# Performance work log

Measured on AMD Instinct MI355X. Metric: run time of the kernel, lower is better.

Reference implementation:

```python
import jax, jax.numpy as jnp
import numpy as np

B, T, C, H = 4, 2048, 1024, 16
HD = C // H


def setup_inputs() -> dict:
    key = jax.random.key(0)
    ks = jax.random.split(key, 9)
    s = 1.0 / np.sqrt(C)
    return {
        "x": jax.random.normal(ks[0], (B, T, C), dtype=jnp.float32),
        "Wk": jax.random.uniform(ks[1], (C, C), jnp.float32, -s, s),
        "bk": jax.random.uniform(ks[2], (C,), jnp.float32, -s, s),
        "Wq": jax.random.uniform(ks[3], (C, C), jnp.float32, -s, s),
        "bq": jax.random.uniform(ks[4], (C,), jnp.float32, -s, s),
        "Wv": jax.random.uniform(ks[5], (C, C), jnp.float32, -s, s),
        "bv": jax.random.uniform(ks[6], (C,), jnp.float32, -s, s),
        "Wp": jax.random.uniform(ks[7], (C, C), jnp.float32, -s, s),
        "bp": jax.random.uniform(ks[8], (C,), jnp.float32, -s, s),
        "padding_mask": jnp.ones((B, T), dtype=jnp.int32),
    }


def reference(x, Wk, bk, Wq, bq, Wv, bv, Wp, bp, padding_mask):
    # torch nn.Linear: y = x @ W.T + b  (W is [out, in])
    def split_heads(t):  # [B,T,C] -> [B,H,T,HD]
        return t.reshape(B, T, H, HD).transpose(0, 2, 1, 3)

    k = split_heads(x @ Wk.T + bk)
    q = split_heads(x @ Wq.T + bq)
    v = split_heads(x @ Wv.T + bv)

    scale = 1.0 / jnp.sqrt(jnp.float32(HD))
    att = jnp.einsum("bhqd,bhkd->bhqk", q, k) * scale  # [B,H,T,T]

    causal = jnp.tril(jnp.ones((T, T), dtype=bool))  # [T,T]
    pad = (padding_mask != 0)[:, None, None, :]       # [B,1,1,T]
    mask = causal[None, None, :, :] & pad
    att = jnp.where(mask, att, -jnp.inf)
    att = jax.nn.softmax(att, axis=-1)

    y = jnp.einsum("bhqk,bhkd->bhqd", att, v)  # [B,H,T,HD]
    y = y.transpose(0, 2, 1, 3).reshape(B, T, C)
    return y @ Wp.T + bp
```

## Files before the change

### kernel.cpp

```cpp
#include <hip/hip_runtime.h>
#include <hip/hip_bf16.h>
#include <math.h>
#include <stdint.h>

#define BB 4
#define TT 2048
#define CC 1024
#define HH 16
#define HD 64
#define MM (BB*TT)
#define NQT2 16
#define SCQ 0.180336878f

using f32x2  = __attribute__((ext_vector_type(2))) float;
using f32x4  = __attribute__((ext_vector_type(4))) float;
using f32x16 = __attribute__((ext_vector_type(16))) float;
using i32x4  = __attribute__((ext_vector_type(4))) int;
using bf16x4 = __attribute__((ext_vector_type(4))) __bf16;
using bf16x8 = __attribute__((ext_vector_type(8))) __bf16;

__device__ __forceinline__ float fast_exp2(float x) {
  return __builtin_amdgcn_exp2f(x);
}

__device__ __forceinline__ int cvt_pk_bf16(float lo, float hi_) {
  int r;
  asm("v_cvt_pk_bf16_f32 %0, %1, %2" : "=v"(r) : "v"(lo), "v"(hi_));
  return r;
}

__device__ __forceinline__ f32x2 max2(f32x2 a, f32x2 b) {
  return __builtin_elementwise_max(a, b);
}

__device__ __forceinline__ void gload_lds16(const void* g, void* l) {
  __builtin_amdgcn_global_load_lds(
      (__attribute__((address_space(1))) void*)(void*)(g),
      (__attribute__((address_space(3))) void*)(l), 16, 0, 0);
}

__global__ __launch_bounds__(256)
void cvt_f32_bf16(const float* __restrict__ s, __bf16* __restrict__ d, int n4) {
  int i = blockIdx.x * 256 + threadIdx.x;
  if (i >= n4) return;
  float4 v = ((const float4*)s)[i];
  bf16x4 o;
  o[0] = (__bf16)v.x; o[1] = (__bf16)v.y; o[2] = (__bf16)v.z; o[3] = (__bf16)v.w;
  *(bf16x4*)(d + (size_t)i * 4) = o;
}

__global__ __launch_bounds__(256)
void cvt_w4(const float* __restrict__ Wq, const float* __restrict__ Wk,
            const float* __restrict__ Wv, const float* __restrict__ Wp,
            __bf16* __restrict__ wqkv, __bf16* __restrict__ wpb) {
  int which = blockIdx.y;
  const float* s = which == 0 ? Wq : which == 1 ? Wk : which == 2 ? Wv : Wp;
  __bf16* d = which == 3 ? wpb : wqkv + (size_t)which * CC * CC;
  float sc = which == 0 ? SCQ : 1.f;
  int i = blockIdx.x * 256 + threadIdx.x;
  float4 v = ((const float4*)s)[i];
  bf16x4 o;
  o[0] = (__bf16)(v.x * sc); o[1] = (__bf16)(v.y * sc);
  o[2] = (__bf16)(v.z * sc); o[3] = (__bf16)(v.w * sc);
  *(bf16x4*)(d + (size_t)i * 4) = o;
}

#define WAITV0 asm volatile("s_waitcnt vmcnt(0)" ::: "memory")
#define SB0    __builtin_amdgcn_sched_barrier(0)

__global__ __launch_bounds__(256, 2)
void gemm_qkv(const __bf16* __restrict__ A, const __bf16* __restrict__ Bm,
              const float* __restrict__ b0, const float* __restrict__ b1,
              const float* __restrict__ b2, __bf16* __restrict__ out,
              __bf16* __restrict__ vt) {
  __shared__ __bf16 U[8448];
  __bf16* As = U;
  __bf16* Bs = U + 4096;
  const int tid = threadIdx.x;
  const int wid = tid >> 6, lane = tid & 63;
  const int g = lane >> 4, lq = lane & 15;
  const int bx0 = blockIdx.x;
  const int bx = (bx0 & 7) * 192 + (bx0 >> 3);
  const int bm = bx / 24, bn = bx % 24;
  const int brow = bm << 7, bcol = bn << 7;
  const int wr = (wid >> 1) << 6, wc = (wid & 1) << 6;

  const int c0 = tid, c1 = tid + 256;
  const int r0 = c0 >> 2, s0_ = (((c0 & 3) - (r0 >> 1)) & 3) << 4;
  const int r1 = c1 >> 2, s1_ = (((c1 & 3) - (r1 >> 1)) & 3) << 4;

  f32x4 acc[4][4] = {};

  for (int kt = 0; kt < CC; kt += 32) {
    __syncthreads();
    gload_lds16((const char*)A + (size_t)(brow + r0) * 2048 + kt * 2 + s0_,
                (char*)As + c0 * 16);
    gload_lds16((const char*)A + (size_t)(brow + r1) * 2048 + kt * 2 + s1_,
                (char*)As + c1 * 16);
    gload_lds16((const char*)Bm + (size_t)(bcol + r0) * 2048 + kt * 2 + s0_,
                (char*)Bs + c0 * 16);
    gload_lds16((const char*)Bm + (size_t)(bcol + r1) * 2048 + kt * 2 + s1_,
                (char*)Bs + c1 * 16);
    __syncthreads();
    bf16x8 av[4], bv[4];
#pragma unroll
    for (int m = 0; m < 4; ++m) {
      int row = wr + m * 16 + lq;
      int sl = (g + (row >> 1)) & 3;
      av[m] = *(const bf16x8*)((const char*)As + row * 64 + sl * 16);
    }
#pragma unroll
    for (int n = 0; n < 4; ++n) {
      int row = wc + n * 16 + lq;
      int sl = (g + (row >> 1)) & 3;
      bv[n] = *(const bf16x8*)((const char*)Bs + row * 64 + sl * 16);
    }
#pragma unroll
    for (int m = 0; m < 4; ++m)
#pragma unroll
      for (int n = 0; n < 4; ++n)
        acc[m][n] = __builtin_amdgcn_mfma_f32_16x16x32_bf16(av[m], bv[n], acc[m][n], 0, 0, 0);
  }

  const int proj = bn >> 3;
  if (proj < 2) {
    const float* bias = proj == 0 ? b0 : b1;
    const float bsc = proj == 0 ? SCQ : 1.f;
#pragma unroll
    for (int n = 0; n < 4; ++n) {
      int col = bcol + wc + n * 16 + lq;
      int cw = col & (CC - 1);
      float bb = bias[cw] * bsc;
      int h_ = cw >> 6, d_ = cw & (HD - 1);
#pragma unroll
      for (int m = 0; m < 4; ++m) {
        int row0 = brow + wr + m * 16 + g * 4;
#pragma unroll
        for (int i = 0; i < 4; ++i) {
          int row = row0 + i;
          int b_ = row >> 11, t_ = row & (TT - 1);
          out[((size_t)proj << 23) +
              ((((size_t)b_ * HH + h_) * TT + t_) << 6) + d_] =
              (__bf16)(acc[m][n][i] + bb);
        }
      }
    }
  } else {
    __syncthreads();
    __bf16* lt = U;
    const int cv0 = (bn & 7) << 7;
    const int b_ = brow >> 11, t0 = brow & (TT - 1);
    const int hbase = (bn & 7) << 1;
    const int rd_d = tid >> 2, rd_tb = (tid & 3) << 5;
#pragma unroll
    for (int cc = 0; cc < 2; ++cc) {
      if ((wid & 1) == cc) {
#pragma unroll
        for (int n = 0; n < 4; ++n) {
          int c = (n << 4) + lq;
          float bb = b2[cv0 + (cc << 6) + c];
#pragma unroll
          for (int m = 0; m < 4; ++m) {
            int r = wr + (m << 4) + (g << 2);
            bf16x4 pk;
#pragma unroll
            for (int i = 0; i < 4; ++i)
              pk[i] = (__bf16)(acc[m][n][i] + bb);
            *(bf16x4*)(lt + c * 130 + r) = pk;
          }
        }
      }
      __syncthreads();
      __bf16* dst = vt + (((size_t)((b_ * HH + hbase + cc) * HD + rd_d)) << 11)
                       + t0 + rd_tb;
      const __bf16* srcl = lt + rd_d * 130 + rd_tb;
#pragma unroll
      for (int j = 0; j < 4; ++j)
        *(bf16x8*)(dst + j * 8) = *(const bf16x8*)(srcl + j * 8);
      __syncthreads();
    }
  }
}

__global__ __launch_bounds__(256, 2)
void gemm_proj(const __bf16* __restrict__ A, const __bf16* __restrict__ Bm,
               const float* __restrict__ bias, float* __restrict__ out,
               int M, int N, int K) {
  __shared__ __bf16 As[128 * 32];
  __shared__ __bf16 Bs[128 * 32];
  const int tid = threadIdx.x;
  const int wid = tid >> 6, lane = tid & 63;
  const int g = lane >> 4, lq = lane & 15;
  const int nbn = N >> 7;
  int bx = blockIdx.x;
  const int nb = gridDim.x;
  if ((nb & 7) == 0) { const int q = nb >> 3; bx = (bx & 7) * q + (bx >> 3); }
  const int brow = (bx / nbn) << 7;
  const int bcol = (bx % nbn) << 7;
  const int wr = (wid >> 1) << 6, wc = (wid & 1) << 6;

  f32x4 acc[4][4] = {};

  const int o0 = wid * 2048 + lane * 16;
  for (int kt = 0; kt < K; kt += 32) {
    __syncthreads();
#pragma unroll
    for (int j = 0; j < 2; ++j) {
      int o = o0 + j * 1024;
      int row = o >> 6, colb = o & 63;
      gload_lds16((const char*)A + ((size_t)(brow + row) * K + kt) * 2 + colb,
                  (char*)As + o);
      gload_lds16((const char*)Bm + ((size_t)(bcol + row) * K + kt) * 2 + colb,
                  (char*)Bs + o);
    }
    __syncthreads();
    bf16x8 av[4], bv[4];
#pragma unroll
    for (int m = 0; m < 4; ++m)
      av[m] = *(const bf16x8*)(As + (wr + m * 16 + lq) * 32 + g * 8);
#pragma unroll
    for (int n = 0; n < 4; ++n)
      bv[n] = *(const bf16x8*)(Bs + (wc + n * 16 + lq) * 32 + g * 8);
#pragma unroll
    for (int m = 0; m < 4; ++m)
#pragma unroll
      for (int n = 0; n < 4; ++n)
        acc[m][n] = __builtin_amdgcn_mfma_f32_16x16x32_bf16(av[m], bv[n], acc[m][n], 0, 0, 0);
  }

#pragma unroll
  for (int m = 0; m < 4; ++m) {
#pragma unroll
    for (int n = 0; n < 4; ++n) {
      int col = bcol + wc + n * 16 + lq;
      float bb = bias[col];
      int row0 = brow + wr + m * 16 + g * 4;
#pragma unroll
      for (int i = 0; i < 4; ++i)
        out[(size_t)(row0 + i) * N + col] = acc[m][n][i] + bb;
    }
  }
}

__global__ __launch_bounds__(256, 4)
void attn_fwd(const __bf16* __restrict__ Q, const __bf16* __restrict__ K,
              const __bf16* __restrict__ Vt, const int* __restrict__ pm,
              __bf16* __restrict__ Y) {
  __shared__ __bf16 Ks[2][64 * 64];
  __shared__ __bf16 Vs[2][64 * 64];
  __shared__ int flg;
  const int tid = threadIdx.x, wid = tid >> 6, lane = tid & 63;
  const int l31 = lane & 31, hi = lane >> 5;
  const int bx = blockIdx.x;
  const int bh = bx & 63, jj = bx >> 6;
  const int qi = 15 - (4 * (jj >> 2) + ((jj + (jj >> 2)) & 3));
  const int b_ = bh >> 4, h_ = bh & 15;
  const __bf16* Qb = Q + (size_t)bh * TT * HD;
  const __bf16* Kb = K + (size_t)bh * TT * HD;
  const __bf16* Vb = Vt + (size_t)bh * HD * TT;
  const int* pmb = pm + b_ * TT;

  const int so = tid * 16;
  const int srow = tid >> 3;
  const int scol = (so & 127) ^ ((srow & 7) << 4);

  const int q0 = qi << 7;
  const int qw = q0 + wid * 32;
  const int ntiles = 2 * qi + 2;
  const int sw0 = (l31 & 7) << 4;

  bf16x8 qf[4];
#pragma unroll
  for (int s = 0; s < 4; ++s)
    qf[s] = *(const bf16x8*)(Qb + (size_t)(qw + l31) * HD + s * 16 + hi * 8);
  SB0;

  int4 pa4 = ((const int4*)pmb)[tid];
  int4 pb4 = ((const int4*)pmb)[tid + 256];
  bool okp = pa4.x && pa4.y && pa4.z && pa4.w &&
             pb4.x && pb4.y && pb4.z && pb4.w;
  if (tid == 0) flg = 1;
  __syncthreads();
  if (!okp) flg = 0;

  {
    char* kd = (char*)&Ks[0][0] + so;
    char* vd = (char*)&Vs[0][0] + so;
#pragma unroll
    for (int j = 0; j < 2; ++j) {
      gload_lds16((const char*)Kb + (size_t)(srow + 32 * j) * 128 + scol,
                  kd + j * 4096);
      gload_lds16((const char*)Vb + (size_t)(srow + 32 * j) * (TT * 2) + scol,
                  vd + j * 4096);
    }
  }
  __syncthreads();
  const bool allones = (flg != 0);

  f32x16 o0 = {}, o1 = {};
  f32x16 vzero = {};
  float lsum = 0.f;
  float m = -INFINITY;

  int cur = 0;
#pragma unroll 1
  for (int t = 0; t < ntiles; ++t) {
    const int kv0 = t << 6;
    WAITV0;
    __builtin_amdgcn_s_barrier(); SB0;
    if (t + 1 < ntiles) {
      char* kd = (char*)&Ks[0][0] + (cur ^ 1) * 8192 + so;
      char* vd = (char*)&Vs[0][0] + (cur ^ 1) * 8192 + so;
      const size_t nk = (size_t)(kv0 + 64);
#pragma unroll
      for (int j = 0; j < 2; ++j) {
        gload_lds16((const char*)Kb + (nk + srow + 32 * j) * 128 + scol,
                    kd + j * 4096);
        gload_lds16((const char*)Vb + (size_t)(srow + 32 * j) * (TT * 2) +
                        nk * 2 + scol,
                    vd + j * 4096);
      }
    }

    unsigned long long bits = ~0ull;
    if (__builtin_expect(!allones, 0))
      bits = __ballot(pmb[kv0 + lane] != 0);

    if (kv0 <= qw + 31) {
      const char* VsC = (const char*)&Vs[0][0] + cur * 8192;

#pragma unroll
      for (int h = 0; h < 2; ++h) {
        const int kvh = kv0 + 32 * h;
        if (kvh <= qw + 31) {
          const char* KsC =
              (const char*)&Ks[0][0] + cur * 8192 + (32 * h + l31) * 128;
          f32x16 S;
          __builtin_amdgcn_s_setprio(1);
          {
            bf16x8 k0 = *(const bf16x8*)(KsC + ((16 * hi) ^ sw0));
            S = __builtin_amdgcn_mfma_f32_32x32x16_bf16(k0, qf[0], vzero, 0, 0, 0);
          }
#pragma unroll
          for (int s = 1; s < 4; ++s) {
            bf16x8 kf = *(const bf16x8*)(KsC + ((32 * s + 16 * hi) ^ sw0));
            S = __builtin_amdgcn_mfma_f32_32x32x16_bf16(kf, qf[s], S, 0, 0, 0);
          }
          __builtin_amdgcn_s_setprio(0);

          if (__builtin_expect(bits != ~0ull, 0)) {
#pragma unroll
            for (int r = 0; r < 16; ++r) {
              const int c = (r & 3) + 8 * (r >> 2);
              if (!((bits >> (32 * h + c + 4 * hi)) & 1ull)) S[r] = -INFINITY;
            }
          }
          if (kvh + 31 > qw) {
            const int thr = qw + l31 - kvh - 4 * hi;
#pragma unroll
            for (int r = 0; r < 16; ++r) {
              const int c = (r & 3) + 8 * (r >> 2);
              S[r] = (c <= thr) ? S[r] : -INFINITY;
            }
          }

          f32x2 x0 = {S[0], S[1]},  x1 = {S[2], S[3]};
          f32x2 x2 = {S[4], S[5]},  x3 = {S[6], S[7]};
          f32x2 x4 = {S[8], S[9]},  x5 = {S[10], S[11]};
          f32x2 x6 = {S[12], S[13]}, x7 = {S[14], S[15]};
          x0 = max2(x0, x4); x1 = max2(x1, x5);
          x2 = max2(x2, x6); x3 = max2(x3, x7);
          x0 = max2(x0, x2); x1 = max2(x1, x3);
          x0 = max2(x0, x1);
          float pmax = fmaxf(x0[0], x0[1]);
          if (!__all(pmax <= m + 8.f)) {
            float nm = fmaxf(pmax, __shfl_xor(pmax, 32));
            float mn = fmaxf(m, nm);
            float c = fast_exp2(m - mn);
            m = mn;
            lsum *= c;
#pragma unroll
            for (int r = 0; r < 16; ++r) {
              float cr = __shfl(c, (r & 3) + 8 * (r >> 2) + 4 * hi);
              o0[r] *= cr;
              o1[r] *= cr;
            }
          }

          const f32x2 mm = {m, m};
#pragma unroll
          for (int r = 0; r < 16; r += 2) {
            f32x2 u = {S[r], S[r + 1]};
            u -= mm;
            S[r] = fast_exp2(u[0]);
            S[r + 1] = fast_exp2(u[1]);
          }
          {
            f32x2 u0 = {S[0], S[1]},  u1 = {S[2], S[3]};
            f32x2 u2 = {S[4], S[5]},  u3 = {S[6], S[7]};
            f32x2 u4 = {S[8], S[9]},  u5 = {S[10], S[11]};
            f32x2 u6 = {S[12], S[13]}, u7 = {S[14], S[15]};
            u0 += u4; u1 += u5; u2 += u6; u3 += u7;
            u0 += u2; u1 += u3;
            u0 += u1;
            lsum += u0[0] + u0[1];
          }

          __builtin_amdgcn_s_setprio(1);
#pragma unroll
          for (int s = 0; s < 2; ++s) {
            int A0 = cvt_pk_bf16(S[8 * s + 0], S[8 * s + 1]);
            int A1 = cvt_pk_bf16(S[8 * s + 2], S[8 * s + 3]);
            int B0 = cvt_pk_bf16(S[8 * s + 4], S[8 * s + 5]);
            int B1 = cvt_pk_bf16(S[8 * s + 6], S[8 * s + 7]);
            int s0 = hi ? A0 : B0, s1 = hi ? A1 : B1;
            int e0 = __shfl_xor(s0, 32), e1 = __shfl_xor(s1, 32);
            i32x4 wv;
            wv[0] = hi ? e0 : A0;
            wv[1] = hi ? e1 : A1;
            wv[2] = hi ? B0 : e0;
            wv[3] = hi ? B1 : e1;
            bf16x8 pa = __builtin_bit_cast(bf16x8, wv);
            const int co = 64 * h + 32 * s + 16 * hi;
            bf16x8 v0 = *(const bf16x8*)(VsC + l31 * 128 + (co ^ sw0));
            bf16x8 v1 = *(const bf16x8*)(VsC + (32 + l31) * 128 + (co ^ sw0));
            o0 = __builtin_amdgcn_mfma_f32_32x32x16_bf16(pa, v0, o0, 0, 0, 0);
            o1 = __builtin_amdgcn_mfma_f32_32x32x16_bf16(pa, v1, o1, 0, 0, 0);
          }
          __builtin_amdgcn_s_setprio(0);
        }
      }
    }
    SB0;
    cur ^= 1;
  }

  float linv = 1.f / (lsum + __shfl_xor(lsum, 32));
#pragma unroll
  for (int r = 0; r < 16; ++r) {
    const int crow = (r & 3) + 8 * (r >> 2) + 4 * hi;
    float ir = __shfl(linv, crow);
    const int qrow = qw + crow;
    __bf16* yp = Y + ((size_t)(b_ * TT + qrow)) * CC + h_ * HD + l31;
    yp[0]  = (__bf16)(o0[r] * ir);
    yp[32] = (__bf16)(o1[r] * ir);
  }
}

extern "C" void kernel_launch(void* const* d_in, const int* in_sizes, int n_in,
                              void* d_out, int out_size, void* d_ws, size_t ws_size,
                              hipStream_t stream) {
  (void)in_sizes; (void)n_in; (void)out_size; (void)ws_size;
  const float* x  = (const float*)d_in[0];
  const float* Wk = (const float*)d_in[1];
  const float* bk = (const float*)d_in[2];
  const float* Wq = (const float*)d_in[3];
  const float* bq = (const float*)d_in[4];
  const float* Wv = (const float*)d_in[5];
  const float* bv = (const float*)d_in[6];
  const float* Wp = (const float*)d_in[7];
  const float* bp = (const float*)d_in[8];
  const int* pmask = (const int*)d_in[9];

  char* ws = (char*)d_ws;
  const size_t MB = 1024 * 1024;
  __bf16* xb   = (__bf16*)(ws);
  __bf16* wqkv = (__bf16*)(ws + 16 * MB);
  __bf16* wpb  = (__bf16*)(ws + 22 * MB);
  __bf16* qb   = (__bf16*)(ws + 24 * MB);
  __bf16* kb   = qb + ((size_t)1 << 23);
  __bf16* vtb  = (__bf16*)(ws + 56 * MB);
  __bf16* yb   = xb;

  int n4 = (MM * CC) / 4;
  cvt_f32_bf16<<<(n4 + 255) / 256, 256, 0, stream>>>(x, xb, n4);
  cvt_w4<<<dim3((CC * CC / 4) / 256, 4), 256, 0, stream>>>(
      Wq, Wk, Wv, Wp, wqkv, wpb);

  gemm_qkv<<<(MM / 128) * (3 * CC / 128), 256, 0, stream>>>(
      xb, wqkv, bq, bk, bv, qb, vtb);

  attn_fwd<<<NQT2 * BB * HH, 256, 0, stream>>>(qb, kb, vtb, pmask, yb);

  gemm_proj<<<(MM / 128) * (CC / 128), 256, 0, stream>>>(
      yb, wpb, bp, (float*)d_out, MM, CC, CC);
}
```

Before: 174.6 us.

## Double-buffer LDS tiles in QKV and projection GEMMs with a single barrier per step

Both GEMM kernels now use two LDS buffers per operand. The next K-slice is issued with direct global-to-LDS loads while MFMAs run on the current one, and each iteration needs only one wait-and-barrier instead of two __syncthreads. The projection GEMM also adopts the swizzled LDS layout and block-index remap from the QKV kernel, and its dimensions are hardcoded. LDS use doubles to 32KB per block, which may affect occupancy and leaves less margin for the epilogue that reuses shared memory.

New measurement: 170.2 us. 2.6% less time.

```diff
diff --git a/kernel.cpp b/kernel.cpp
--- a/kernel.cpp
+++ b/kernel.cpp
@@ -66,6 +66,7 @@
 }
 
 #define WAITV0 asm volatile("s_waitcnt vmcnt(0)" ::: "memory")
+#define BARR   __builtin_amdgcn_s_barrier()
 #define SB0    __builtin_amdgcn_sched_barrier(0)
 
 __global__ __launch_bounds__(256, 2)
@@ -73,9 +74,8 @@
               const float* __restrict__ b0, const float* __restrict__ b1,
               const float* __restrict__ b2, __bf16* __restrict__ out,
               __bf16* __restrict__ vt) {
-  __shared__ __bf16 U[8448];
-  __bf16* As = U;
-  __bf16* Bs = U + 4096;
+  __shared__ __bf16 U[16384];
+  char* Ub = (char*)U;
   const int tid = threadIdx.x;
   const int wid = tid >> 6, lane = tid & 63;
   const int g = lane >> 4, lq = lane & 15;
@@ -88,39 +88,53 @@
   const int c0 = tid, c1 = tid + 256;
   const int r0 = c0 >> 2, s0_ = (((c0 & 3) - (r0 >> 1)) & 3) << 4;
   const int r1 = c1 >> 2, s1_ = (((c1 & 3) - (r1 >> 1)) & 3) << 4;
+  const char* Ag = (const char*)A;
+  const char* Bg = (const char*)Bm;
+
+#define STAGEQ(ko, buf)                                                       \
+  {                                                                           \
+    gload_lds16(Ag + (size_t)(brow + r0) * 2048 + (ko) + s0_,                 \
+                Ub + (buf) * 8192 + c0 * 16);                                 \
+    gload_lds16(Ag + (size_t)(brow + r1) * 2048 + (ko) + s1_,                 \
+                Ub + (buf) * 8192 + c1 * 16);                                 \
+    gload_lds16(Bg + (size_t)(bcol + r0) * 2048 + (ko) + s0_,                 \
+                Ub + 16384 + (buf) * 8192 + c0 * 16);                         \
+    gload_lds16(Bg + (size_t)(bcol + r1) * 2048 + (ko) + s1_,                 \
+                Ub + 16384 + (buf) * 8192 + c1 * 16);                         \
+  }
 
   f32x4 acc[4][4] = {};
 
-  for (int kt = 0; kt < CC; kt += 32) {
-    __syncthreads();
-    gload_lds16((const char*)A + (size_t)(brow + r0) * 2048 + kt * 2 + s0_,
-                (char*)As + c0 * 16);
-    gload_lds16((const char*)A + (size_t)(brow + r1) * 2048 + kt * 2 + s1_,
-                (char*)As + c1 * 16);
-    gload_lds16((const char*)Bm + (size_t)(bcol + r0) * 2048 + kt * 2 + s0_,
-                (char*)Bs + c0 * 16);
-    gload_lds16((const char*)Bm + (size_t)(bcol + r1) * 2048 + kt * 2 + s1_,
-                (char*)Bs + c1 * 16);
-    __syncthreads();
+  STAGEQ(0, 0);
+  int cur = 0;
+#pragma unroll 1
+  for (int t = 0; t < 32; ++t) {
+    WAITV0; BARR; SB0;
+    if (t + 1 < 32) STAGEQ((t + 1) << 6, cur ^ 1);
+    const char* Ac = Ub + cur * 8192;
+    const char* Bc = Ub + 16384 + cur * 8192;
     bf16x8 av[4], bv[4];
 #pragma unroll
     for (int m = 0; m < 4; ++m) {
       int row = wr + m * 16 + lq;
       int sl = (g + (row >> 1)) & 3;
-      av[m] = *(const bf16x8*)((const char*)As + row * 64 + sl * 16);
+      av[m] = *(const bf16x8*)(Ac + row * 64 + sl * 16);
     }
 #pragma unroll
     for (int n = 0; n < 4; ++n) {
       int row = wc + n * 16 + lq;
       int sl = (g + (row >> 1)) & 3;
-      bv[n] = *(const bf16x8*)((const char*)Bs + row * 64 + sl * 16);
+      bv[n] = *(const bf16x8*)(Bc + row * 64 + sl * 16);
     }
 #pragma unroll
     for (int m = 0; m < 4; ++m)
 #pragma unroll
       for (int n = 0; n < 4; ++n)
         acc[m][n] = __builtin_amdgcn_mfma_f32_16x16x32_bf16(av[m], bv[n], acc[m][n], 0, 0, 0);
-  }
+    SB0;
+    cur ^= 1;
+  }
+#undef STAGEQ
 
   const int proj = bn >> 3;
   if (proj < 2) {
@@ -184,49 +198,68 @@
 
 __global__ __launch_bounds__(256, 2)
 void gemm_proj(const __bf16* __restrict__ A, const __bf16* __restrict__ Bm,
-               const float* __restrict__ bias, float* __restrict__ out,
-               int M, int N, int K) {
-  __shared__ __bf16 As[128 * 32];
-  __shared__ __bf16 Bs[128 * 32];
+               const float* __restrict__ bias, float* __restrict__ out) {
+  __shared__ __bf16 U[16384];
+  char* Ub = (char*)U;
   const int tid = threadIdx.x;
   const int wid = tid >> 6, lane = tid & 63;
   const int g = lane >> 4, lq = lane & 15;
-  const int nbn = N >> 7;
-  int bx = blockIdx.x;
-  const int nb = gridDim.x;
-  if ((nb & 7) == 0) { const int q = nb >> 3; bx = (bx & 7) * q + (bx >> 3); }
-  const int brow = (bx / nbn) << 7;
-  const int bcol = (bx % nbn) << 7;
+  const int bx0 = blockIdx.x;
+  const int bx = (bx0 & 7) * 64 + (bx0 >> 3);
+  const int brow = (bx >> 3) << 7;
+  const int bcol = (bx & 7) << 7;
   const int wr = (wid >> 1) << 6, wc = (wid & 1) << 6;
 
+  const int c0 = tid, c1 = tid + 256;
+  const int r0 = c0 >> 2, s0_ = (((c0 & 3) - (r0 >> 1)) & 3) << 4;
+  const int r1 = c1 >> 2, s1_ = (((c1 & 3) - (r1 >> 1)) & 3) << 4;
+  const char* Ag = (const char*)A;
+  const char* Bg = (const char*)Bm;
+
+#define STAGEP(ko, buf)                                                       \
+  {                                                                           \
+    gload_lds16(Ag + (size_t)(brow + r0) * 2048 + (ko) + s0_,                 \
+                Ub + (buf) * 8192 + c0 * 16);                                 \
+    gload_lds16(Ag + (size_t)(brow + r1) * 2048 + (ko) + s1_,                 \
+                Ub + (buf) * 8192 + c1 * 16);                                 \
+    gload_lds16(Bg + (size_t)(bcol + r0) * 2048 + (ko) + s0_,                 \
+                Ub + 16384 + (buf) * 8192 + c0 * 16);                         \
+    gload_lds16(Bg + (size_t)(bcol + r1) * 2048 + (ko) + s1_,                 \
+                Ub + 16384 + (buf) * 8192 + c1 * 16);                         \
+  }
+
   f32x4 acc[4][4] = {};
 
-  const int o0 = wid * 2048 + lane * 16;
-  for (int kt = 0; kt < K; kt += 32) {
-    __syncthreads();
-#pragma unroll
-    for (int j = 0; j < 2; ++j) {
-      int o = o0 + j * 1024;
-      int row = o >> 6, colb = o & 63;
-      gload_lds16((const char*)A + ((size_t)(brow + row) * K + kt) * 2 + colb,
-                  (char*)As + o);
-      gload_lds16((const char*)Bm + ((size_t)(bcol + row) * K + kt) * 2 + colb,
-                  (char*)Bs + o);
-    }
-    __syncthreads();
+  STAGEP(0, 0);
+  int cur = 0;
+#pragma unroll 1
+  for (int t = 0; t < 32; ++t) {
+    WAITV0; BARR; SB0;
+    if (t + 1 < 32) STAGEP((t + 1) << 6, cur ^ 1);
+    const char* Ac = Ub + cur * 8192;
+    const char* Bc = Ub + 16384 + cur * 8192;
     bf16x8 av[4], bv[4];
 #pragma unroll
-    for (int m = 0; m < 4; ++m)
-      av[m] = *(const bf16x8*)(As + (wr + m * 16 + lq) * 32 + g * 8);
-#pragma unroll
-    for (int n = 0; n < 4; ++n)
-      bv[n] = *(const bf16x8*)(Bs + (wc + n * 16 + lq) * 32 + g * 8);
+    for (int m = 0; m < 4; ++m) {
+      int row = wr + m * 16 + lq;
+      int sl = (g + (row >> 1)) & 3;
+      av[m] = *(const bf16x8*)(Ac + row * 64 + sl * 16);
+    }
+#pragma unroll
+    for (int n = 0; n < 4; ++n) {
+      int row = wc + n * 16 + lq;
+      int sl = (g + (row >> 1)) & 3;
+      bv[n] = *(const bf16x8*)(Bc + row * 64 + sl * 16);
+    }
 #pragma unroll
     for (int m = 0; m < 4; ++m)
 #pragma unroll
       for (int n = 0; n < 4; ++n)
         acc[m][n] = __builtin_amdgcn_mfma_f32_16x16x32_bf16(av[m], bv[n], acc[m][n], 0, 0, 0);
-  }
+    SB0;
+    cur ^= 1;
+  }
+#undef STAGEP
 
 #pragma unroll
   for (int m = 0; m < 4; ++m) {
@@ -237,7 +270,7 @@
       int row0 = brow + wr + m * 16 + g * 4;
 #pragma unroll
       for (int i = 0; i < 4; ++i)
-        out[(size_t)(row0 + i) * N + col] = acc[m][n][i] + bb;
+        out[(size_t)(row0 + i) * CC + col] = acc[m][n][i] + bb;
     }
   }
 }
@@ -483,5 +516,5 @@
   attn_fwd<<<NQT2 * BB * HH, 256, 0, stream>>>(qb, kb, vtb, pmask, yb);
 
   gemm_proj<<<(MM / 128) * (CC / 128), 256, 0, stream>>>(
-      yb, wpb, bp, (float*)d_out, MM, CC, CC);
-}
+      yb, wpb, bp, (float*)d_out);
+}
```
